# Performance work log

Hardware: AMD Instinct MI355X
Metric: run time of the kernel (lower is better)

The kernel has to match this reference:

```python
import jax, jax.numpy as jnp
import numpy as np

TOPK = 32  # init kwarg topk=32, method='softmax'


def setup_inputs() -> dict:
    key = jax.random.key(0)
    k1, k2 = jax.random.split(key)
    X1 = jax.random.normal(k1, (8192, 64), dtype=jnp.float32)
    X2 = jax.random.normal(k2, (8192, 64), dtype=jnp.float32)
    return {"X1": X1, "X2": X2}


def reference(X1, X2):
    # pairwise Euclidean distance via the matmul expansion (same math as torch.cdist p=2)
    sq = (
        jnp.sum(X1 * X1, axis=-1)[:, None]
        + jnp.sum(X2 * X2, axis=-1)[None, :]
        - 2.0 * (X1 @ X2.T)
    )  # [N1, N2]
    neg_dist = -jnp.sqrt(jnp.maximum(sq, 0.0))
    # top-k along dim=1, softmax over the k selected values
    val, idx = jax.lax.top_k(neg_dist, TOPK)          # [N1, K]
    score = jax.nn.softmax(val, axis=1)               # [N1, K]
    # scatter scores back into a dense zero matrix
    rows = jnp.arange(neg_dist.shape[0])[:, None]     # [N1, 1]
    out = jnp.zeros_like(neg_dist).at[rows, idx].set(score)
    return out, score
```

## Files before the change

kernel.cpp:

```cpp
#include <hip/hip_runtime.h>
#include <math.h>
#include <float.h>
#include <limits.h>

#define N 8192
#define D 64
#define TOPK 32
#define TILE 128
#define CAP 1024

__device__ __forceinline__ unsigned ford(float f) {
    unsigned u = __float_as_uint(f);
    return u ^ ((u & 0x80000000u) ? 0xFFFFFFFFu : 0x80000000u);
}
__device__ __forceinline__ float finv(unsigned u) {
    unsigned b = (u & 0x80000000u) ? (u ^ 0x80000000u) : ~u;
    return __uint_as_float(b);
}

__global__ __launch_bounds__(256) void norms_kernel(
    const float* __restrict__ X1, const float* __restrict__ X2,
    float* __restrict__ nrm)
{
    int id = blockIdx.x * blockDim.x + threadIdx.x;
    if (id >= 2 * N) return;
    const float* X = (id < N) ? X1 : X2;
    int r = (id < N) ? id : id - N;
    const float4* p = (const float4*)(X + (size_t)r * D);
    float s = 0.f;
#pragma unroll
    for (int q = 0; q < D / 4; ++q) {
        float4 v = p[q];
        s += v.x * v.x + v.y * v.y + v.z * v.z + v.w * v.w;
    }
    nrm[id] = s;
}

__global__ __launch_bounds__(256, 2) void dist_kernel(
    const float* __restrict__ X1, const float* __restrict__ X2,
    const float* __restrict__ nrm, float* __restrict__ out,
    float* __restrict__ tmax, int have_tmax)
{
    __shared__ float As[D * TILE];
    __shared__ float Bs[D * TILE];

    const int t = threadIdx.x;
    const int row0 = blockIdx.y * TILE;
    const int col0 = blockIdx.x * TILE;

#pragma unroll
    for (int p = 0; p < 8; ++p) {
        int lin = p * 256 + t;
        int r   = lin >> 4;
        int d4  = (lin & 15) << 2;
        int g   = (d4 >> 2) & 7;
        int cb  = r ^ (g << 3);
        float4 a = *(const float4*)(X1 + (size_t)(row0 + r) * D + d4);
        As[(d4 + 0) * TILE + cb] = a.x;
        As[(d4 + 1) * TILE + cb] = a.y;
        As[(d4 + 2) * TILE + cb] = a.z;
        As[(d4 + 3) * TILE + cb] = a.w;
        float4 b = *(const float4*)(X2 + (size_t)(col0 + r) * D + d4);
        Bs[(d4 + 0) * TILE + cb] = b.x;
        Bs[(d4 + 1) * TILE + cb] = b.y;
        Bs[(d4 + 2) * TILE + cb] = b.z;
        Bs[(d4 + 3) * TILE + cb] = b.w;
    }
    __syncthreads();

    const int tx = t & 15;
    const int ty = t >> 4;
    float acc[8][8] = {};

#pragma unroll 8
    for (int k = 0; k < D; ++k) {
        int gk  = (k >> 2) & 7;
        int ab  = k * TILE + ((ty ^ gk) << 3);
        int bb0 = k * TILE + ((4 * tx) ^ (gk << 3));
        float4 a0 = *(const float4*)&As[ab];
        float4 a1 = *(const float4*)&As[ab + 4];
        float4 b0 = *(const float4*)&Bs[bb0];
        float4 b1 = *(const float4*)&Bs[bb0 + 64];
        float av[8] = {a0.x, a0.y, a0.z, a0.w, a1.x, a1.y, a1.z, a1.w};
        float bv[8] = {b0.x, b0.y, b0.z, b0.w, b1.x, b1.y, b1.z, b1.w};
#pragma unroll
        for (int i = 0; i < 8; ++i)
#pragma unroll
            for (int j = 0; j < 8; ++j)
                acc[i][j] += av[i] * bv[j];
    }

    float na[8], nb[8];
#pragma unroll
    for (int i = 0; i < 8; ++i) na[i] = nrm[row0 + 8 * ty + i];
#pragma unroll
    for (int q = 0; q < 4; ++q) {
        nb[q]     = nrm[N + col0 + 4 * tx + q];
        nb[4 + q] = nrm[N + col0 + 64 + 4 * tx + q];
    }

    float rmax[8];
#pragma unroll
    for (int i = 0; i < 8; ++i) rmax[i] = -FLT_MAX;

#pragma unroll
    for (int i = 0; i < 8; ++i) {
        float* po = out + (size_t)(row0 + 8 * ty + i) * N + col0 + 4 * tx;
        float4 o0, o1;
        float* f0 = (float*)&o0;
        float* f1 = (float*)&o1;
#pragma unroll
        for (int q = 0; q < 4; ++q) {
            float s0 = na[i] + nb[q] - 2.0f * acc[i][q];
            f0[q] = -fmaxf(s0, 0.0f);
            float s1 = na[i] + nb[4 + q] - 2.0f * acc[i][4 + q];
            f1[q] = -fmaxf(s1, 0.0f);
            rmax[i] = fmaxf(rmax[i], fmaxf(f0[q], f1[q]));
        }
        *(float4*)po        = o0;
        *(float4*)(po + 64) = o1;
    }

    if (have_tmax) {
#pragma unroll
        for (int i = 0; i < 8; ++i) {
            float mv = rmax[i];
            mv = fmaxf(mv, __shfl_down(mv, 8, 16));
            mv = fmaxf(mv, __shfl_down(mv, 4, 16));
            mv = fmaxf(mv, __shfl_down(mv, 2, 16));
            mv = fmaxf(mv, __shfl_down(mv, 1, 16));
            if (tx == 0)
                tmax[(size_t)(row0 + 8 * ty + i) * 64 + blockIdx.x] = mv;
        }
    }
}

__global__ __launch_bounds__(256) void topk_kernel(
    float* __restrict__ out, float* __restrict__ score_out,
    const float* __restrict__ tmax, int have_tmax)
{
    __shared__ unsigned long long cand[4][CAP];
    __shared__ int scnt[4];

    const int t    = threadIdx.x;
    const int w    = t >> 6;
    const int lane = t & 63;
    const int r    = blockIdx.x * 4 + w;
    float* row = out + (size_t)r * N;
    const float4* row4 = (const float4*)row;

    float thr;
    float lm = -FLT_MAX;
    if (have_tmax) {
        float tm = tmax[(size_t)r * 64 + lane];
        unsigned km = ford(tm);
        int rk = 0;
#pragma unroll
        for (int l = 0; l < 64; ++l) {
            unsigned o = __shfl(km, l);
            rk += (o > km || (o == km && l < lane)) ? 1 : 0;
        }
        unsigned long long bm = __ballot(rk == 31);
        thr = __shfl(tm, __ffsll(bm) - 1);
    } else {
#pragma unroll 8
        for (int c = 0; c < 32; ++c) {
            float4 x = row4[c * 64 + lane];
            lm = fmaxf(lm, fmaxf(fmaxf(x.x, x.y), fmaxf(x.z, x.w)));
        }
        thr = lm;
        for (int off = 32; off > 0; off >>= 1)
            thr = fminf(thr, __shfl_xor(thr, off));
    }

    for (int attempt = 0; ; ++attempt) {
        if (lane == 0) scnt[w] = 0;
        __builtin_amdgcn_s_waitcnt(0xC07F);
        for (int c = 0; c < 32; ++c) {
            float4 x = row4[c * 64 + lane];
            float vs[4] = {x.x, x.y, x.z, x.w};
#pragma unroll
            for (int q = 0; q < 4; ++q) {
                float v = vs[q];
                lm = fmaxf(lm, v);
                if (v >= thr) {
                    int p = atomicAdd(&scnt[w], 1);
                    if (p < CAP) {
                        unsigned long long key =
                            ((unsigned long long)ford(v) << 32) |
                            (unsigned)(8191 - (4 * (c * 64 + lane) + q));
                        cand[w][p] = key;
                    }
                }
            }
        }
        __builtin_amdgcn_s_waitcnt(0xC07F);
        if (scnt[w] <= CAP || attempt == 1) break;
        unsigned kml = ford(lm);
        int rk2 = 0;
#pragma unroll
        for (int l = 0; l < 64; ++l) {
            unsigned o = __shfl(kml, l);
            rk2 += (o < kml || (o == kml && l < lane)) ? 1 : 0;
        }
        unsigned long long bm2 = __ballot(rk2 == 15);
        float t2 = __shfl(lm, __ffsll(bm2) - 1);
        thr = fmaxf(thr, t2);
    }
    const int n = min(scnt[w], CAP);

    unsigned long long mykey = 0ull;
    for (int it = 0; it < TOPK; ++it) {
        unsigned long long b = 0ull; int bp = 0;
        for (int q = lane; q < n; q += 64) {
            unsigned long long kk = cand[w][q];
            if (kk > b) { b = kk; bp = q; }
        }
        for (int off = 32; off > 0; off >>= 1) {
            unsigned long long ob = __shfl_down(b, off);
            int op = __shfl_down(bp, off);
            if (ob > b) { b = ob; bp = op; }
        }
        unsigned long long b0 = __shfl(b, 0);
        int bp0 = __shfl(bp, 0);
        if (lane == it) { mykey = b0; cand[w][bp0] = 0ull; }
    }

    float myv = 0.f; int myj = 0;
    if (lane < TOPK) {
        float sv = finv((unsigned)(mykey >> 32));
        myv = -sqrtf(-sv);
        myj = 8191 - (int)(mykey & 0xFFFFFFFFu);
    }
    float Mx = __shfl(myv, 0);
    float e = (lane < TOPK) ? expf(myv - Mx) : 0.f;
    float Z = e;
    for (int off = 32; off > 0; off >>= 1) Z += __shfl_xor(Z, off);
    float s = e / Z;
    if (lane < TOPK) score_out[(size_t)r * TOPK + lane] = s;

    const float4 zz = make_float4(0.f, 0.f, 0.f, 0.f);
#pragma unroll 8
    for (int c = 0; c < 32; ++c) ((float4*)row)[c * 64 + lane] = zz;
    __builtin_amdgcn_s_waitcnt(0x0F70);
    if (lane < TOPK) row[myj] = s;
}

extern "C" void kernel_launch(void* const* d_in, const int* in_sizes, int n_in,
                              void* d_out, int out_size, void* d_ws, size_t ws_size,
                              hipStream_t stream)
{
    const float* X1 = (const float*)d_in[0];
    const float* X2 = (const float*)d_in[1];
    float* out = (float*)d_out;
    float* nrm = (float*)d_ws;
    float* tmax = nrm + 2 * N;
    size_t need = (size_t)(2 * N + (size_t)N * 64) * sizeof(float);
    int have_tmax = (ws_size >= need) ? 1 : 0;

    norms_kernel<<<(2 * N + 255) / 256, 256, 0, stream>>>(X1, X2, nrm);

    dim3 grid(N / TILE, N / TILE);
    dist_kernel<<<grid, 256, 0, stream>>>(X1, X2, nrm, out, tmax, have_tmax);

    topk_kernel<<<N / 4, 256, 0, stream>>>(out, out + (size_t)N * N, tmax, have_tmax);
}
```

Before: 476.9 us.

## Write distances to workspace and scan only qualifying column tiles in top-k

When the workspace is large enough, the distance matrix goes to a separate buffer and a dedicated kernel zeros the output. The top-k pass then reads only the 128-column tiles whose per-tile max reaches the 32nd-largest tile max, not the full row, and writes the scores into the pre-zeroed output. This cuts the top-k read traffic but adds a full-size workspace write plus a separate zeroing pass, so total memory traffic may not fall. The fallback path also drops the retry logic that handled candidate-buffer overflow.

```diff
diff --git a/kernel.cpp b/kernel.cpp
--- a/kernel.cpp
+++ b/kernel.cpp
@@ -16,6 +16,15 @@
 __device__ __forceinline__ float finv(unsigned u) {
     unsigned b = (u & 0x80000000u) ? (u ^ 0x80000000u) : ~u;
     return __uint_as_float(b);
+}
+
+__global__ __launch_bounds__(256) void zero_kernel(float4* __restrict__ p)
+{
+    const int n4 = N * N / 4;
+    const float4 zz = make_float4(0.f, 0.f, 0.f, 0.f);
+    int stride = gridDim.x * 256;
+    for (int i = blockIdx.x * 256 + threadIdx.x; i < n4; i += stride)
+        p[i] = zz;
 }
 
 __global__ __launch_bounds__(256) void norms_kernel(
@@ -38,7 +47,7 @@
 
 __global__ __launch_bounds__(256, 2) void dist_kernel(
     const float* __restrict__ X1, const float* __restrict__ X2,
-    const float* __restrict__ nrm, float* __restrict__ out,
+    const float* __restrict__ nrm, float* __restrict__ dst,
     float* __restrict__ tmax, int have_tmax)
 {
     __shared__ float As[D * TILE];
@@ -105,7 +114,7 @@
 
 #pragma unroll
     for (int i = 0; i < 8; ++i) {
-        float* po = out + (size_t)(row0 + 8 * ty + i) * N + col0 + 4 * tx;
+        float* po = dst + (size_t)(row0 + 8 * ty + i) * N + col0 + 4 * tx;
         float4 o0, o1;
         float* f0 = (float*)&o0;
         float* f1 = (float*)&o1;
@@ -136,21 +145,22 @@
 }
 
 __global__ __launch_bounds__(256) void topk_kernel(
-    float* __restrict__ out, float* __restrict__ score_out,
-    const float* __restrict__ tmax, int have_tmax)
+    const float* __restrict__ src, float* __restrict__ out,
+    float* __restrict__ score_out, const float* __restrict__ tmax,
+    int have_tmax, int fastmode)
 {
     __shared__ unsigned long long cand[4][CAP];
+    __shared__ int qlist[4][64];
     __shared__ int scnt[4];
 
     const int t    = threadIdx.x;
     const int w    = t >> 6;
     const int lane = t & 63;
     const int r    = blockIdx.x * 4 + w;
-    float* row = out + (size_t)r * N;
-    const float4* row4 = (const float4*)row;
+    const float*  rowsrc = src + (size_t)r * N;
+    const float4* row4   = (const float4*)rowsrc;
 
     float thr;
-    float lm = -FLT_MAX;
     if (have_tmax) {
         float tm = tmax[(size_t)r * 64 + lane];
         unsigned km = ford(tm);
@@ -161,8 +171,40 @@
             rk += (o > km || (o == km && l < lane)) ? 1 : 0;
         }
         unsigned long long bm = __ballot(rk == 31);
-        thr = __shfl(tm, __ffsll(bm) - 1);
+        thr = __shfl(tm, __ffsll((long long)bm) - 1);
+
+        bool qual = fastmode ? (tm >= thr) : true;
+        unsigned long long qm = __ballot(qual);
+        int nqq = __popcll(qm);
+        if (qual) {
+            int pos = __popcll(qm & ((lane == 0) ? 0ull : (~0ull >> (64 - lane))));
+            qlist[w][pos] = lane;
+        }
+        if (lane == 0) scnt[w] = 0;
+        __builtin_amdgcn_s_waitcnt(0xC07F);
+
+        for (int m = 0; m < nqq; m += 2) {
+            int slot = m + (lane >> 5);
+            bool valid = slot < nqq;
+            int tile = qlist[w][valid ? slot : m];
+            float4 x = row4[tile * 32 + (lane & 31)];
+            float vs[4] = {x.x, x.y, x.z, x.w};
+#pragma unroll
+            for (int q = 0; q < 4; ++q) {
+                float v = vs[q];
+                if (valid && v >= thr) {
+                    int p = atomicAdd(&scnt[w], 1);
+                    if (p < CAP) {
+                        int j = tile * 128 + 4 * (lane & 31) + q;
+                        cand[w][p] = ((unsigned long long)ford(v) << 32) |
+                                     (unsigned)(8191 - j);
+                    }
+                }
+            }
+        }
+        __builtin_amdgcn_s_waitcnt(0xC07F);
     } else {
+        float lm = -FLT_MAX;
 #pragma unroll 8
         for (int c = 0; c < 32; ++c) {
             float4 x = row4[c * 64 + lane];
@@ -171,9 +213,6 @@
         thr = lm;
         for (int off = 32; off > 0; off >>= 1)
             thr = fminf(thr, __shfl_xor(thr, off));
-    }
-
-    for (int attempt = 0; ; ++attempt) {
         if (lane == 0) scnt[w] = 0;
         __builtin_amdgcn_s_waitcnt(0xC07F);
         for (int c = 0; c < 32; ++c) {
@@ -182,30 +221,17 @@
 #pragma unroll
             for (int q = 0; q < 4; ++q) {
                 float v = vs[q];
-                lm = fmaxf(lm, v);
                 if (v >= thr) {
                     int p = atomicAdd(&scnt[w], 1);
                     if (p < CAP) {
-                        unsigned long long key =
-                            ((unsigned long long)ford(v) << 32) |
-                            (unsigned)(8191 - (4 * (c * 64 + lane) + q));
-                        cand[w][p] = key;
+                        int j = 4 * (c * 64 + lane) + q;
+                        cand[w][p] = ((unsigned long long)ford(v) << 32) |
+                                     (unsigned)(8191 - j);
                     }
                 }
             }
         }
         __builtin_amdgcn_s_waitcnt(0xC07F);
-        if (scnt[w] <= CAP || attempt == 1) break;
-        unsigned kml = ford(lm);
-        int rk2 = 0;
-#pragma unroll
-        for (int l = 0; l < 64; ++l) {
-            unsigned o = __shfl(kml, l);
-            rk2 += (o < kml || (o == kml && l < lane)) ? 1 : 0;
-        }
-        unsigned long long bm2 = __ballot(rk2 == 15);
-        float t2 = __shfl(lm, __ffsll(bm2) - 1);
-        thr = fmaxf(thr, t2);
     }
     const int n = min(scnt[w], CAP);
 
@@ -239,11 +265,14 @@
     float s = e / Z;
     if (lane < TOPK) score_out[(size_t)r * TOPK + lane] = s;
 
-    const float4 zz = make_float4(0.f, 0.f, 0.f, 0.f);
+    float* rowout = out + (size_t)r * N;
+    if (!fastmode) {
+        const float4 zz = make_float4(0.f, 0.f, 0.f, 0.f);
 #pragma unroll 8
-    for (int c = 0; c < 32; ++c) ((float4*)row)[c * 64 + lane] = zz;
-    __builtin_amdgcn_s_waitcnt(0x0F70);
-    if (lane < TOPK) row[myj] = s;
+        for (int c = 0; c < 32; ++c) ((float4*)rowout)[c * 64 + lane] = zz;
+        __builtin_amdgcn_s_waitcnt(0x0F70);
+    }
+    if (lane < TOPK) rowout[myj] = s;
 }
 
 extern "C" void kernel_launch(void* const* d_in, const int* in_sizes, int n_in,
@@ -252,16 +281,26 @@
 {
     const float* X1 = (const float*)d_in[0];
     const float* X2 = (const float*)d_in[1];
-    float* out = (float*)d_out;
-    float* nrm = (float*)d_ws;
+    float* out  = (float*)d_out;
+    float* nrm  = (float*)d_ws;
     float* tmax = nrm + 2 * N;
-    size_t need = (size_t)(2 * N + (size_t)N * 64) * sizeof(float);
-    int have_tmax = (ws_size >= need) ? 1 : 0;
+    float* dmat = tmax + (size_t)N * 64;
+
+    size_t need_tmax = (size_t)(2 * N + (size_t)N * 64) * sizeof(float);
+    size_t need_full = need_tmax + (size_t)N * N * sizeof(float);
+    int have_tmax = (ws_size >= need_tmax) ? 1 : 0;
+    int fastmode  = (ws_size >= need_full) ? 1 : 0;
+
+    float* dst = fastmode ? dmat : out;
 
     norms_kernel<<<(2 * N + 255) / 256, 256, 0, stream>>>(X1, X2, nrm);
 
     dim3 grid(N / TILE, N / TILE);
-    dist_kernel<<<grid, 256, 0, stream>>>(X1, X2, nrm, out, tmax, have_tmax);
-
-    topk_kernel<<<N / 4, 256, 0, stream>>>(out, out + (size_t)N * N, tmax, have_tmax);
-}
+    dist_kernel<<<grid, 256, 0, stream>>>(X1, X2, nrm, dst, tmax, have_tmax);
+
+    if (fastmode)
+        zero_kernel<<<4096, 256, 0, stream>>>((float4*)out);
+
+    topk_kernel<<<N / 4, 256, 0, stream>>>(dst, out, out + (size_t)N * N,
+                                           tmax, have_tmax, fastmode);
+}
```

Result: slower. 512.6 us (+7.5%).
